# Kernel tuning notes

Hardware: AMD Instinct MI355X
Metric: run time of the kernel (lower is better)

Reference implementation:

```python
import jax, jax.numpy as jnp
import numpy as np

N_JOINTS = 17
NEG_INF = -9e15
BN_EPS = 1e-5


def _chain_adjacency(n):
    # skeleton-like chain adjacency with self loops (stand-in for the pose skeleton adj)
    a = np.eye(n, dtype=np.float32)
    idx = np.arange(n - 1)
    a[idx, idx + 1] = 1.0
    a[idx + 1, idx] = 1.0
    return jnp.asarray(a)


def setup_inputs() -> dict:
    key = jax.random.key(0)
    ks = jax.random.split(key, 6)
    B, D, T, N = 32, 128, 512, N_JOINTS
    H, hd = 16, D // 16  # 16 heads, head_dim 8
    s = 1.0 / np.sqrt(D)
    return {
        "x": jax.random.normal(ks[0], (B, D, T, N), dtype=jnp.float32),
        "adj": _chain_adjacency(N),
        "Wq": jax.random.normal(ks[1], (H, D, hd), dtype=jnp.float32) * s,
        "Wk": jax.random.normal(ks[2], (H, D, hd), dtype=jnp.float32) * s,
        "Wv": jax.random.normal(ks[3], (H, D, hd), dtype=jnp.float32) * s,
        "adj2": jnp.full((H, N, N), 1e-6, dtype=jnp.float32),
        "conv_w": jax.random.normal(ks[4], (2 * D, 2 * D), dtype=jnp.float32) * (1.0 / np.sqrt(2 * D)),
        "bn_gamma": jnp.ones((2 * D,), dtype=jnp.float32),
        "bn_beta": jnp.zeros((2 * D,), dtype=jnp.float32),
        "bn_mean": jnp.zeros((2 * D,), dtype=jnp.float32),
        "bn_var": jnp.ones((2 * D,), dtype=jnp.float32),
    }


def reference(x, adj, Wq, Wk, Wv, adj2, conv_w, bn_gamma, bn_beta, bn_mean, bn_var):
    hd = Wq.shape[-1]
    xp = jnp.transpose(x, (0, 2, 3, 1))                      # (B,T,N,D)
    # multi-head adjacency-masked graph attention (MultiGlobalGraph)
    q = jnp.einsum('btnd,hde->bhtne', xp, Wq)
    k = jnp.einsum('btnd,hde->bhtne', xp, Wk)
    v = jnp.einsum('btnd,hde->bhtne', xp, Wv)
    e = jnp.einsum('bhtne,bhtme->bhtnm', q, k) / jnp.sqrt(jnp.asarray(hd, xp.dtype))
    a = adj[None, :, :] + adj2                               # (H,N,N) learnable adj offset
    a = 0.5 * (a + jnp.swapaxes(a, -1, -2))                  # symmetrize
    mask = a > 0
    e = jnp.where(mask[None, :, None, :, :], e, jnp.asarray(NEG_INF, e.dtype))
    attn = jax.nn.softmax(e, axis=-1)                        # (B,H,T,N,N)
    out = jnp.einsum('bhtnm,bhtme->bhtne', attn, v)
    B, H, T, N, _ = out.shape
    out = jnp.transpose(out, (0, 2, 3, 1, 4)).reshape(B, T, N, H * hd)
    # residual concat + conv1x1 + BN(eval) + ReLU
    cat = jnp.concatenate([xp, out], axis=-1)                # (B,T,N,2D)
    y = jnp.einsum('btnc,oc->btno', cat, conv_w)
    y = (y - bn_mean) * jax.lax.rsqrt(bn_var + BN_EPS) * bn_gamma + bn_beta
    y = jax.nn.relu(y)
    return jnp.transpose(y, (0, 3, 1, 2))                    # (B,2D,T,N)
```

## Files before the change

kernel.cpp:

```cpp
#include <hip/hip_runtime.h>
#include <hip/hip_bf16.h>
#include <math.h>

#define NJ 17
#define DD 128
#define TT 512
#define HH 16
#define CC 256
#define NEG_INF -9e15f

typedef __attribute__((ext_vector_type(8))) short short8;
typedef __attribute__((ext_vector_type(4))) float floatx4;
typedef _Float16 h8 __attribute__((ext_vector_type(8)));
typedef _Float16 h2 __attribute__((ext_vector_type(2)));

#define WB_CONV 0
#define WB_QKV  131072
#define WB_MOFF 229376
#define WB_BIAS 247872
#define PREP_ITEMS (65536 + 49152 + 4624 + 256)

__global__ __launch_bounds__(256) void prep_kernel(
        const float* __restrict__ adj,
        const float* __restrict__ wq,
        const float* __restrict__ wk,
        const float* __restrict__ wv,
        const float* __restrict__ adj2,
        const float* __restrict__ conv_w,
        const float* __restrict__ gamma,
        const float* __restrict__ beta,
        const float* __restrict__ mean,
        const float* __restrict__ var,
        char* __restrict__ ws) {
    int g = blockIdx.x * 256 + threadIdx.x;
    if (g < 65536) {
        int j = g & 7, lane = (g >> 3) & 63, kn = g >> 9;
        int ks = kn & 7, nt = kn >> 3;
        int o = nt * 16 + (lane & 15);
        int c = ks * 32 + ((lane >> 4) & 3) * 8 + j;
        float sg = gamma[o] * rsqrtf(var[o] + 1e-5f);
        ((__hip_bfloat16*)(ws + WB_CONV))[g] = __float2bfloat16(conv_w[o * CC + c] * sg);
        return;
    }
    g -= 65536;
    if (g < 49152) {
        int j = g & 7, lane = (g >> 3) & 63, kn = g >> 9;
        int ks = kn & 3, nt = kn >> 2;
        int n = nt * 16 + (lane & 15);
        int k = ks * 32 + ((lane >> 4) & 3) * 8 + j;
        int mat = n >> 7;
        int wcol = n & 127;
        int h = wcol >> 3, e = wcol & 7;
        const float* src = (mat == 0) ? wq : ((mat == 1) ? wk : wv);
        float v = src[(h * DD + k) * 8 + e];
        if (mat == 0) v *= 0.35355339059327373f;
        ((__hip_bfloat16*)(ws + WB_QKV))[g] = __float2bfloat16(v);
        return;
    }
    g -= 49152;
    if (g < HH * NJ * NJ) {
        int h = g / (NJ * NJ);
        int r = g - h * NJ * NJ;
        int n = r / NJ, m = r - n * NJ;
        float a1 = adj[n * NJ + m] + adj2[(h * NJ + n) * NJ + m];
        float a2 = adj[m * NJ + n] + adj2[(h * NJ + m) * NJ + n];
        ((float*)(ws + WB_MOFF))[g] = (0.5f * (a1 + a2) > 0.f) ? 0.f : NEG_INF;
        return;
    }
    g -= HH * NJ * NJ;
    if (g < CC) {
        float sg = gamma[g] * rsqrtf(var[g] + 1e-5f);
        ((float*)(ws + WB_BIAS))[g] = beta[g] - mean[g] * sg;
    }
}

#define CAT_STRIDE 264
#define LDS_CAT_BYTES (34 * CAT_STRIDE * 2)
#define LDS_TOTAL (LDS_CAT_BYTES + 2 * 34 * 128 * 2)

__global__ __launch_bounds__(512, 2) void gab_main(
        const float* __restrict__ x,
        const char* __restrict__ ws,
        float* __restrict__ out) {
    const int tp = blockIdx.x;
    const int t0 = 2 * ((tp & 7) * 32 + (tp >> 3));
    const int b = blockIdx.y;
    const int tid = threadIdx.x;
    const int lane = tid & 63;
    const int wave = tid >> 6;
    const int l15 = lane & 15;
    const int lq = lane >> 4;

    __shared__ __align__(16) char smem[LDS_TOTAL];
    __hip_bfloat16 (*cat)[CAT_STRIDE] = (__hip_bfloat16 (*)[CAT_STRIDE])smem;
    _Float16 (*kv)[34][128] = (_Float16 (*)[34][128])(smem + LDS_CAT_BYTES);

    const float* xb = x + (size_t)b * DD * TT * NJ + (size_t)t0 * NJ;
    for (int i = tid; i < DD * 17; i += 512) {
        int d = i / 17;
        int j = 2 * (i - d * 17);
        float2 f = *(const float2*)(xb + (size_t)d * (TT * NJ) + j);
        cat[j][d] = __float2bfloat16(f.x);
        cat[j + 1][d] = __float2bfloat16(f.y);
    }
    __syncthreads();

    {
        const short8* bbase = (const short8*)(ws + WB_QKV);
        const int nt0 = wave * 3;
        for (int i = 0; i < 3; ++i) {
            const int nt = nt0 + i;
            floatx4 acc0 = {0.f, 0.f, 0.f, 0.f}, acc1 = acc0, acc2 = acc0;
            const short8* bp = bbase + (nt * 4) * 64 + lane;
#pragma unroll
            for (int ks = 0; ks < 4; ++ks) {
                short8 bf = bp[ks * 64];
                const int k0 = ks * 32 + lq * 8;
                short8 a0 = *(const short8*)&cat[l15][k0];
                short8 a1 = *(const short8*)&cat[16 + l15][k0];
                short8 a2 = *(const short8*)&cat[32 + l15][k0];
                acc0 = __builtin_amdgcn_mfma_f32_16x16x32_bf16(a0, bf, acc0, 0, 0, 0);
                acc1 = __builtin_amdgcn_mfma_f32_16x16x32_bf16(a1, bf, acc1, 0, 0, 0);
                acc2 = __builtin_amdgcn_mfma_f32_16x16x32_bf16(a2, bf, acc2, 0, 0, 0);
            }
            const int col = nt * 16 + l15;
            const int mat = col >> 7;
            const int mc = col & 127;
            const int rbase = lq * 4;
            if (mat == 0) {
                _Float16* qd = (_Float16*)smem + 128 + mc;
#pragma unroll
                for (int r = 0; r < 4; ++r) {
                    qd[(rbase + r) * CAT_STRIDE] = (_Float16)acc0[r];
                    qd[(16 + rbase + r) * CAT_STRIDE] = (_Float16)acc1[r];
                    int row2 = 32 + rbase + r;
                    if (row2 < 34) qd[row2 * CAT_STRIDE] = (_Float16)acc2[r];
                }
            } else {
                _Float16* kd = &kv[mat - 1][0][mc];
#pragma unroll
                for (int r = 0; r < 4; ++r) {
                    kd[(rbase + r) * 128] = (_Float16)acc0[r];
                    kd[(16 + rbase + r) * 128] = (_Float16)acc1[r];
                    int row2 = 32 + rbase + r;
                    if (row2 < 34) kd[row2 * 128] = (_Float16)acc2[r];
                }
            }
        }
    }
    __syncthreads();

    {
        const float* moff = (const float*)(ws + WB_MOFF);
        for (int it = tid; it < 2 * HH * NJ; it += 512) {
            const int t = it / (HH * NJ);
            const int r2 = it - t * (HH * NJ);
            const int h = r2 / NJ;
            const int n = r2 - h * NJ;
            const int row = t * NJ + n;
            const float* mo = moff + (h * NJ + n) * NJ;
            const h8 qv = *(const h8*)((const _Float16*)smem + row * CAT_STRIDE + 128 + h * 8);
            const h2* q2 = (const h2*)&qv;
            const _Float16* kbase = &kv[0][t * NJ][h * 8];
            const _Float16* vbase = &kv[1][t * NJ][h * 8];
            float sum = 0.f;
            float ov[8];
#pragma unroll
            for (int e = 0; e < 8; ++e) ov[e] = 0.f;
#pragma unroll
            for (int m = 0; m < NJ; ++m) {
                const h8 kvec = *(const h8*)(kbase + m * 128);
                float a = mo[m];
#if __has_builtin(__builtin_amdgcn_fdot2)
                const h2* k2 = (const h2*)&kvec;
                a = __builtin_amdgcn_fdot2(q2[0], k2[0], a, false);
                a = __builtin_amdgcn_fdot2(q2[1], k2[1], a, false);
                a = __builtin_amdgcn_fdot2(q2[2], k2[2], a, false);
                a = __builtin_amdgcn_fdot2(q2[3], k2[3], a, false);
#else
#pragma unroll
                for (int e = 0; e < 8; ++e) a += (float)qv[e] * (float)kvec[e];
#endif
                const float p = __expf(a);
                sum += p;
                const h8 vvec = *(const h8*)(vbase + m * 128);
#pragma unroll
                for (int e = 0; e < 8; ++e) ov[e] += p * (float)vvec[e];
            }
            const float inv = 1.0f / sum;
            __hip_bfloat16 tmp[8];
#pragma unroll
            for (int e = 0; e < 8; ++e) tmp[e] = __float2bfloat16(ov[e] * inv);
            *(short8*)((__hip_bfloat16*)smem + row * CAT_STRIDE + 128 + h * 8) = *(short8*)tmp;
        }
    }
    __syncthreads();

    {
        const short8* cbase = (const short8*)(ws + WB_CONV);
        const float* biasp = (const float*)(ws + WB_BIAS);
        const int nt0 = wave * 2;
        for (int i = 0; i < 2; ++i) {
            const int nt = nt0 + i;
            floatx4 acc0 = {0.f, 0.f, 0.f, 0.f}, acc1 = acc0, acc2 = acc0;
            const short8* bp = cbase + (nt * 8) * 64 + lane;
#pragma unroll
            for (int ks = 0; ks < 8; ++ks) {
                short8 bf = bp[ks * 64];
                const int k0 = ks * 32 + lq * 8;
                short8 a0 = *(const short8*)&cat[l15][k0];
                short8 a1 = *(const short8*)&cat[16 + l15][k0];
                short8 a2 = *(const short8*)&cat[32 + l15][k0];
                acc0 = __builtin_amdgcn_mfma_f32_16x16x32_bf16(a0, bf, acc0, 0, 0, 0);
                acc1 = __builtin_amdgcn_mfma_f32_16x16x32_bf16(a1, bf, acc1, 0, 0, 0);
                acc2 = __builtin_amdgcn_mfma_f32_16x16x32_bf16(a2, bf, acc2, 0, 0, 0);
            }
            const int o = nt * 16 + l15;
            const float bias = biasp[o];
            const size_t ob = ((size_t)b * CC + o) * (TT * NJ) + (size_t)t0 * NJ;
            const int rbase = lq * 4;
#pragma unroll
            for (int r = 0; r < 4; ++r) {
                out[ob + rbase + r] = fmaxf(acc0[r] + bias, 0.f);
                out[ob + 16 + rbase + r] = fmaxf(acc1[r] + bias, 0.f);
                int row2 = 32 + rbase + r;
                if (row2 < 34) out[ob + row2] = fmaxf(acc2[r] + bias, 0.f);
            }
        }
    }
}

extern "C" void kernel_launch(void* const* d_in, const int* in_sizes, int n_in,
                              void* d_out, int out_size, void* d_ws, size_t ws_size,
                              hipStream_t stream) {
    const float* x      = (const float*)d_in[0];
    const float* adj    = (const float*)d_in[1];
    const float* wq     = (const float*)d_in[2];
    const float* wk     = (const float*)d_in[3];
    const float* wv     = (const float*)d_in[4];
    const float* adj2   = (const float*)d_in[5];
    const float* conv_w = (const float*)d_in[6];
    const float* gamma  = (const float*)d_in[7];
    const float* beta   = (const float*)d_in[8];
    const float* mean   = (const float*)d_in[9];
    const float* var    = (const float*)d_in[10];
    char* ws   = (char*)d_ws;
    float* outp = (float*)d_out;

    const int B = in_sizes[0] / (DD * TT * NJ);

    prep_kernel<<<(PREP_ITEMS + 255) / 256, 256, 0, stream>>>(
        adj, wq, wk, wv, adj2, conv_w, gamma, beta, mean, var, ws);

    dim3 grid(TT / 2, B);
    gab_main<<<grid, 512, 0, stream>>>(x, ws, outp);
}
```

Baseline: 612.2 us.

## Pad KV LDS, bitmask adjacency, exp2 softmax, widen loads, interleave MFMA tiles

Several changes at once. The adjacency mask becomes a per-row bitmask instead of a float offset table. The softmax uses exp2, with log2(e) folded into the Q weights. The x staging loads become float4, and the K/V LDS rows are padded to avoid bank conflicts. The QKV and conv MFMA loops are unrolled across two N tiles so A fragments are reused, and launch bounds request 4 blocks per CU. The aim is to cut global mask reads, LDS conflicts and redundant LDS A loads, and to raise occupancy, at the cost of register pressure from the larger accumulator set under tighter launch bounds.

```diff
diff --git a/kernel.cpp b/kernel.cpp
--- a/kernel.cpp
+++ b/kernel.cpp
@@ -11,6 +11,8 @@
 
 typedef __attribute__((ext_vector_type(8))) short short8;
 typedef __attribute__((ext_vector_type(4))) float floatx4;
+typedef __attribute__((ext_vector_type(4), aligned(4))) float float4u;
+typedef __attribute__((ext_vector_type(2), aligned(4))) float float2u;
 typedef _Float16 h8 __attribute__((ext_vector_type(8)));
 typedef _Float16 h2 __attribute__((ext_vector_type(2)));
 
@@ -18,7 +20,7 @@
 #define WB_QKV  131072
 #define WB_MOFF 229376
 #define WB_BIAS 247872
-#define PREP_ITEMS (65536 + 49152 + 4624 + 256)
+#define PREP_ITEMS (65536 + 49152 + 272 + 256)
 
 __global__ __launch_bounds__(256) void prep_kernel(
         const float* __restrict__ adj,
@@ -53,21 +55,23 @@
         int h = wcol >> 3, e = wcol & 7;
         const float* src = (mat == 0) ? wq : ((mat == 1) ? wk : wv);
         float v = src[(h * DD + k) * 8 + e];
-        if (mat == 0) v *= 0.35355339059327373f;
+        if (mat == 0) v *= 0.35355339059327373f * 1.4426950408889634f;
         ((__hip_bfloat16*)(ws + WB_QKV))[g] = __float2bfloat16(v);
         return;
     }
     g -= 49152;
-    if (g < HH * NJ * NJ) {
-        int h = g / (NJ * NJ);
-        int r = g - h * NJ * NJ;
-        int n = r / NJ, m = r - n * NJ;
-        float a1 = adj[n * NJ + m] + adj2[(h * NJ + n) * NJ + m];
-        float a2 = adj[m * NJ + n] + adj2[(h * NJ + m) * NJ + n];
-        ((float*)(ws + WB_MOFF))[g] = (0.5f * (a1 + a2) > 0.f) ? 0.f : NEG_INF;
+    if (g < HH * NJ) {
+        int h = g / NJ, n = g - h * NJ;
+        unsigned bits = 0;
+        for (int m = 0; m < NJ; ++m) {
+            float a1 = adj[n * NJ + m] + adj2[(h * NJ + n) * NJ + m];
+            float a2 = adj[m * NJ + n] + adj2[(h * NJ + m) * NJ + n];
+            if (0.5f * (a1 + a2) > 0.f) bits |= (1u << m);
+        }
+        ((unsigned*)(ws + WB_MOFF))[g] = bits;
         return;
     }
-    g -= HH * NJ * NJ;
+    g -= HH * NJ;
     if (g < CC) {
         float sg = gamma[g] * rsqrtf(var[g] + 1e-5f);
         ((float*)(ws + WB_BIAS))[g] = beta[g] - mean[g] * sg;
@@ -75,10 +79,11 @@
 }
 
 #define CAT_STRIDE 264
+#define KV_STRIDE 136
 #define LDS_CAT_BYTES (34 * CAT_STRIDE * 2)
-#define LDS_TOTAL (LDS_CAT_BYTES + 2 * 34 * 128 * 2)
-
-__global__ __launch_bounds__(512, 2) void gab_main(
+#define LDS_TOTAL (LDS_CAT_BYTES + 2 * 34 * KV_STRIDE * 2)
+
+__global__ __launch_bounds__(512, 4) void gab_main(
         const float* __restrict__ x,
         const char* __restrict__ ws,
         float* __restrict__ out) {
@@ -93,36 +98,33 @@
 
     __shared__ __align__(16) char smem[LDS_TOTAL];
     __hip_bfloat16 (*cat)[CAT_STRIDE] = (__hip_bfloat16 (*)[CAT_STRIDE])smem;
-    _Float16 (*kv)[34][128] = (_Float16 (*)[34][128])(smem + LDS_CAT_BYTES);
+    _Float16 (*kv)[34][KV_STRIDE] = (_Float16 (*)[34][KV_STRIDE])(smem + LDS_CAT_BYTES);
 
     const float* xb = x + (size_t)b * DD * TT * NJ + (size_t)t0 * NJ;
-    for (int i = tid; i < DD * 17; i += 512) {
-        int d = i / 17;
-        int j = 2 * (i - d * 17);
-        float2 f = *(const float2*)(xb + (size_t)d * (TT * NJ) + j);
-        cat[j][d] = __float2bfloat16(f.x);
-        cat[j + 1][d] = __float2bfloat16(f.y);
+    for (int i = tid; i < DD * 9; i += 512) {
+        int d = i / 9;
+        int c = i - d * 9;
+        const float* src = xb + (size_t)d * (TT * NJ);
+        if (c < 8) {
+            float4u f = *(const float4u*)(src + 4 * c);
+            int j = 4 * c;
+            cat[j][d]     = __float2bfloat16(f.x);
+            cat[j + 1][d] = __float2bfloat16(f.y);
+            cat[j + 2][d] = __float2bfloat16(f.z);
+            cat[j + 3][d] = __float2bfloat16(f.w);
+        } else {
+            float2u f = *(const float2u*)(src + 32);
+            cat[32][d] = __float2bfloat16(f.x);
+            cat[33][d] = __float2bfloat16(f.y);
+        }
     }
     __syncthreads();
 
     {
         const short8* bbase = (const short8*)(ws + WB_QKV);
         const int nt0 = wave * 3;
-        for (int i = 0; i < 3; ++i) {
-            const int nt = nt0 + i;
-            floatx4 acc0 = {0.f, 0.f, 0.f, 0.f}, acc1 = acc0, acc2 = acc0;
-            const short8* bp = bbase + (nt * 4) * 64 + lane;
-#pragma unroll
-            for (int ks = 0; ks < 4; ++ks) {
-                short8 bf = bp[ks * 64];
-                const int k0 = ks * 32 + lq * 8;
-                short8 a0 = *(const short8*)&cat[l15][k0];
-                short8 a1 = *(const short8*)&cat[16 + l15][k0];
-                short8 a2 = *(const short8*)&cat[32 + l15][k0];
-                acc0 = __builtin_amdgcn_mfma_f32_16x16x32_bf16(a0, bf, acc0, 0, 0, 0);
-                acc1 = __builtin_amdgcn_mfma_f32_16x16x32_bf16(a1, bf, acc1, 0, 0, 0);
-                acc2 = __builtin_amdgcn_mfma_f32_16x16x32_bf16(a2, bf, acc2, 0, 0, 0);
-            }
+
+        auto store_qkv = [&](int nt, const floatx4& v0, const floatx4& v1, const floatx4& v2) {
             const int col = nt * 16 + l15;
             const int mat = col >> 7;
             const int mc = col & 127;
@@ -131,34 +133,73 @@
                 _Float16* qd = (_Float16*)smem + 128 + mc;
 #pragma unroll
                 for (int r = 0; r < 4; ++r) {
-                    qd[(rbase + r) * CAT_STRIDE] = (_Float16)acc0[r];
-                    qd[(16 + rbase + r) * CAT_STRIDE] = (_Float16)acc1[r];
+                    qd[(rbase + r) * CAT_STRIDE] = (_Float16)v0[r];
+                    qd[(16 + rbase + r) * CAT_STRIDE] = (_Float16)v1[r];
                     int row2 = 32 + rbase + r;
-                    if (row2 < 34) qd[row2 * CAT_STRIDE] = (_Float16)acc2[r];
+                    if (row2 < 34) qd[row2 * CAT_STRIDE] = (_Float16)v2[r];
                 }
             } else {
                 _Float16* kd = &kv[mat - 1][0][mc];
 #pragma unroll
                 for (int r = 0; r < 4; ++r) {
-                    kd[(rbase + r) * 128] = (_Float16)acc0[r];
-                    kd[(16 + rbase + r) * 128] = (_Float16)acc1[r];
+                    kd[(rbase + r) * KV_STRIDE] = (_Float16)v0[r];
+                    kd[(16 + rbase + r) * KV_STRIDE] = (_Float16)v1[r];
                     int row2 = 32 + rbase + r;
-                    if (row2 < 34) kd[row2 * 128] = (_Float16)acc2[r];
+                    if (row2 < 34) kd[row2 * KV_STRIDE] = (_Float16)v2[r];
                 }
             }
+        };
+
+        {
+            floatx4 acc[2][3];
+#pragma unroll
+            for (int u = 0; u < 2; ++u)
+#pragma unroll
+                for (int m = 0; m < 3; ++m) acc[u][m] = (floatx4){0.f, 0.f, 0.f, 0.f};
+#pragma unroll
+            for (int ks = 0; ks < 4; ++ks) {
+                const int k0 = ks * 32 + lq * 8;
+                short8 a0 = *(const short8*)&cat[l15][k0];
+                short8 a1 = *(const short8*)&cat[16 + l15][k0];
+                short8 a2 = *(const short8*)&cat[32 + l15][k0];
+#pragma unroll
+                for (int u = 0; u < 2; ++u) {
+                    short8 bf = bbase[((nt0 + u) * 4 + ks) * 64 + lane];
+                    acc[u][0] = __builtin_amdgcn_mfma_f32_16x16x32_bf16(a0, bf, acc[u][0], 0, 0, 0);
+                    acc[u][1] = __builtin_amdgcn_mfma_f32_16x16x32_bf16(a1, bf, acc[u][1], 0, 0, 0);
+                    acc[u][2] = __builtin_amdgcn_mfma_f32_16x16x32_bf16(a2, bf, acc[u][2], 0, 0, 0);
+                }
+            }
+            store_qkv(nt0, acc[0][0], acc[0][1], acc[0][2]);
+            store_qkv(nt0 + 1, acc[1][0], acc[1][1], acc[1][2]);
+        }
+        {
+            floatx4 acc0 = {0.f, 0.f, 0.f, 0.f}, acc1 = acc0, acc2 = acc0;
+#pragma unroll
+            for (int ks = 0; ks < 4; ++ks) {
+                const int k0 = ks * 32 + lq * 8;
+                short8 a0 = *(const short8*)&cat[l15][k0];
+                short8 a1 = *(const short8*)&cat[16 + l15][k0];
+                short8 a2 = *(const short8*)&cat[32 + l15][k0];
+                short8 bf = bbase[((nt0 + 2) * 4 + ks) * 64 + lane];
+                acc0 = __builtin_amdgcn_mfma_f32_16x16x32_bf16(a0, bf, acc0, 0, 0, 0);
+                acc1 = __builtin_amdgcn_mfma_f32_16x16x32_bf16(a1, bf, acc1, 0, 0, 0);
+                acc2 = __builtin_amdgcn_mfma_f32_16x16x32_bf16(a2, bf, acc2, 0, 0, 0);
+            }
+            store_qkv(nt0 + 2, acc0, acc1, acc2);
         }
     }
     __syncthreads();
 
     {
-        const float* moff = (const float*)(ws + WB_MOFF);
+        const unsigned* mbits = (const unsigned*)(ws + WB_MOFF);
         for (int it = tid; it < 2 * HH * NJ; it += 512) {
             const int t = it / (HH * NJ);
             const int r2 = it - t * (HH * NJ);
             const int h = r2 / NJ;
             const int n = r2 - h * NJ;
             const int row = t * NJ + n;
-            const float* mo = moff + (h * NJ + n) * NJ;
+            const unsigned bits = mbits[h * NJ + n];
             const h8 qv = *(const h8*)((const _Float16*)smem + row * CAT_STRIDE + 128 + h * 8);
             const h2* q2 = (const h2*)&qv;
             const _Float16* kbase = &kv[0][t * NJ][h * 8];
@@ -169,8 +210,8 @@
             for (int e = 0; e < 8; ++e) ov[e] = 0.f;
 #pragma unroll
             for (int m = 0; m < NJ; ++m) {
-                const h8 kvec = *(const h8*)(kbase + m * 128);
-                float a = mo[m];
+                const h8 kvec = *(const h8*)(kbase + m * KV_STRIDE);
+                float a = 0.f;
 #if __has_builtin(__builtin_amdgcn_fdot2)
                 const h2* k2 = (const h2*)&kvec;
                 a = __builtin_amdgcn_fdot2(q2[0], k2[0], a, false);
@@ -181,9 +222,14 @@
 #pragma unroll
                 for (int e = 0; e < 8; ++e) a += (float)qv[e] * (float)kvec[e];
 #endif
-                const float p = __expf(a);
+                a = ((bits >> m) & 1u) ? a : NEG_INF;
+#if __has_builtin(__builtin_amdgcn_exp2f)
+                const float p = __builtin_amdgcn_exp2f(a);
+#else
+                const float p = __expf(a * 0.6931471805599453f);
+#endif
                 sum += p;
-                const h8 vvec = *(const h8*)(vbase + m * 128);
+                const h8 vvec = *(const h8*)(vbase + m * KV_STRIDE);
 #pragma unroll
                 for (int e = 0; e < 8; ++e) ov[e] += p * (float)vvec[e];
             }
@@ -200,31 +246,37 @@
         const short8* cbase = (const short8*)(ws + WB_CONV);
         const float* biasp = (const float*)(ws + WB_BIAS);
         const int nt0 = wave * 2;
-        for (int i = 0; i < 2; ++i) {
-            const int nt = nt0 + i;
-            floatx4 acc0 = {0.f, 0.f, 0.f, 0.f}, acc1 = acc0, acc2 = acc0;
-            const short8* bp = cbase + (nt * 8) * 64 + lane;
-#pragma unroll
-            for (int ks = 0; ks < 8; ++ks) {
-                short8 bf = bp[ks * 64];
-                const int k0 = ks * 32 + lq * 8;
-                short8 a0 = *(const short8*)&cat[l15][k0];
-                short8 a1 = *(const short8*)&cat[16 + l15][k0];
-                short8 a2 = *(const short8*)&cat[32 + l15][k0];
-                acc0 = __builtin_amdgcn_mfma_f32_16x16x32_bf16(a0, bf, acc0, 0, 0, 0);
-                acc1 = __builtin_amdgcn_mfma_f32_16x16x32_bf16(a1, bf, acc1, 0, 0, 0);
-                acc2 = __builtin_amdgcn_mfma_f32_16x16x32_bf16(a2, bf, acc2, 0, 0, 0);
-            }
-            const int o = nt * 16 + l15;
+        floatx4 acc[2][3];
+#pragma unroll
+        for (int u = 0; u < 2; ++u)
+#pragma unroll
+            for (int m = 0; m < 3; ++m) acc[u][m] = (floatx4){0.f, 0.f, 0.f, 0.f};
+#pragma unroll
+        for (int ks = 0; ks < 8; ++ks) {
+            const int k0 = ks * 32 + lq * 8;
+            short8 a0 = *(const short8*)&cat[l15][k0];
+            short8 a1 = *(const short8*)&cat[16 + l15][k0];
+            short8 a2 = *(const short8*)&cat[32 + l15][k0];
+#pragma unroll
+            for (int u = 0; u < 2; ++u) {
+                short8 bf = cbase[((nt0 + u) * 8 + ks) * 64 + lane];
+                acc[u][0] = __builtin_amdgcn_mfma_f32_16x16x32_bf16(a0, bf, acc[u][0], 0, 0, 0);
+                acc[u][1] = __builtin_amdgcn_mfma_f32_16x16x32_bf16(a1, bf, acc[u][1], 0, 0, 0);
+                acc[u][2] = __builtin_amdgcn_mfma_f32_16x16x32_bf16(a2, bf, acc[u][2], 0, 0, 0);
+            }
+        }
+#pragma unroll
+        for (int u = 0; u < 2; ++u) {
+            const int o = (nt0 + u) * 16 + l15;
             const float bias = biasp[o];
             const size_t ob = ((size_t)b * CC + o) * (TT * NJ) + (size_t)t0 * NJ;
             const int rbase = lq * 4;
 #pragma unroll
             for (int r = 0; r < 4; ++r) {
-                out[ob + rbase + r] = fmaxf(acc0[r] + bias, 0.f);
-                out[ob + 16 + rbase + r] = fmaxf(acc1[r] + bias, 0.f);
+                out[ob + rbase + r] = fmaxf(acc[u][0][r] + bias, 0.f);
+                out[ob + 16 + rbase + r] = fmaxf(acc[u][1][r] + bias, 0.f);
                 int row2 = 32 + rbase + r;
-                if (row2 < 34) out[ob + row2] = fmaxf(acc2[r] + bias, 0.f);
+                if (row2 < 34) out[ob + row2] = fmaxf(acc[u][2][r] + bias, 0.f);
             }
         }
     }
```

Result: faster. 579.3 us (-5.4%).
